# Kernel tuning notes

Hardware: AMD Instinct MI355X
Metric: run time of the kernel (lower is better)

The kernel has to match this reference:

```python
import jax, jax.numpy as jnp
import numpy as np
from jax import lax

B, C, H, W = 8, 64, 112, 112
MID = 256
K = 5
DIL = 2
PAD = 4


def setup_inputs() -> dict:
    key = jax.random.key(0)
    k1, k2, k3, k4, k5 = jax.random.split(key, 5)
    x = jax.random.normal(k1, (B, C, H, W), dtype=jnp.float32)
    # conv1: in_channel -> 256, k=5, dilation=2, pad=4
    w1 = jax.random.normal(k2, (MID, C, K, K), dtype=jnp.float32) * (1.0 / np.sqrt(C * K * K))
    b1 = jax.random.normal(k3, (MID,), dtype=jnp.float32) * 0.01
    # conv2: 256 -> 25, 1x1
    w2 = jax.random.normal(k4, (K * K, MID, 1, 1), dtype=jnp.float32) * (1.0 / np.sqrt(MID))
    b2 = jax.random.normal(k5, (K * K,), dtype=jnp.float32) * 0.01
    return {"x": x, "w1": w1, "b1": b1, "w2": w2, "b2": b2}


def reference(x, w1, b1, w2, b2):
    # attention-weight branch
    k = lax.conv_general_dilated(
        x, w1, window_strides=(1, 1), padding=[(PAD, PAD), (PAD, PAD)],
        rhs_dilation=(DIL, DIL), dimension_numbers=("NCHW", "OIHW", "NCHW"))
    k = k + b1[None, :, None, None]                       # [B, 256, H, W]
    k = jnp.einsum("oi,bihw->bohw", w2[:, :, 0, 0], k) + b2[None, :, None, None]
    k = jax.nn.softmax(k, axis=1)                          # [B, 25, H, W]

    # fused local attention: weighted sum over the 5x5 dilated neighborhood.
    # Equivalent to unfold(x, k=5, dilation=2, pad=4) * k summed over the 25 taps,
    # but never materializes the [B, C, 25, H, W] unfolded tensor.
    xp = jnp.pad(x, ((0, 0), (0, 0), (PAD, PAD), (PAD, PAD)))
    out = jnp.zeros_like(x)
    for idx in range(K * K):
        i, j = divmod(idx, K)
        patch = lax.dynamic_slice(xp, (0, 0, DIL * i, DIL * j), (B, C, H, W))
        out = out + patch * k[:, idx:idx + 1]              # broadcast over C
    return out
```

## Files before the change

kernel.cpp:

```cpp
#include <hip/hip_runtime.h>

#define BATCH 8
#define CH    64
#define HH    112
#define WW    112
#define HW    (HH * WW)
#define NP    (BATCH * HW)
#define TAPS  25
#define MIDC  256
#define PIX   64
#define CPW   16
#define NBLK  (NP / PIX)
#define NXCD  8
#define CPX   (NBLK / NXCD)

#define WEFF_N   (CH * TAPS * TAPS)
#define WEFF_TOT (WEFF_N + TAPS)
__global__ __launch_bounds__(256) void weff_kernel(
    const float* __restrict__ w1, const float* __restrict__ b1,
    const float* __restrict__ w2, const float* __restrict__ b2,
    float* __restrict__ weff, float* __restrict__ beff) {
  __shared__ float part[3][64];
  const int lane  = threadIdx.x & 63;
  const int chunk = threadIdx.x >> 6;
  const int id    = blockIdx.x * 64 + lane;

  float acc = 0.f;
  if (id < WEFF_N) {
    const int tap = id % TAPS;
    const int t2  = id / TAPS;
    const int o   = t2 % TAPS;
    const int c   = t2 / TAPS;
    const float* w2o = w2 + o * MIDC + chunk * 64;
    const float* w1p = w1 + ((size_t)(chunk * 64) * CH + c) * TAPS + tap;
    float a0 = 0.f, a1 = 0.f;
    #pragma unroll 8
    for (int m = 0; m < 64; m += 2) {
      a0 = fmaf(w1p[(size_t)m       * CH * TAPS], w2o[m],     a0);
      a1 = fmaf(w1p[(size_t)(m + 1) * CH * TAPS], w2o[m + 1], a1);
    }
    acc = a0 + a1;
  } else if (id < WEFF_TOT) {
    const int o = id - WEFF_N;
    const float* w2o = w2 + o * MIDC + chunk * 64;
    const float* b1p = b1 + chunk * 64;
    #pragma unroll 8
    for (int m = 0; m < 64; ++m) acc = fmaf(w2o[m], b1p[m], acc);
  }

  if (chunk) part[chunk - 1][lane] = acc;
  __syncthreads();
  if (chunk == 0 && id < WEFF_TOT) {
    float r = acc + part[0][lane] + part[1][lane] + part[2][lane];
    if (id < WEFF_N) {
      const int tap = id % TAPS;
      const int t2  = id / TAPS;
      const int o   = t2 % TAPS;
      const int c   = t2 / TAPS;
      weff[(c * TAPS + tap) * TAPS + o] = r;
    } else {
      beff[id - WEFF_N] = r + b2[id - WEFF_N];
    }
  }
}

__global__ __launch_bounds__(256, 6) void picanet_main(
    const float* __restrict__ x, const float* __restrict__ weff,
    const float* __restrict__ beff, float* __restrict__ out) {
  __shared__ float red[2 * PIX * TAPS];

  const int lane = threadIdx.x & 63;
  const int wave = threadIdx.x >> 6;
  const int c0 = __builtin_amdgcn_readfirstlane(wave * CPW);

  const int lb = (blockIdx.x & (NXCD - 1)) * CPX + (blockIdx.x >> 3);
  const int p  = lb * PIX + lane;
  const int b  = p / HW;
  const int hw = p % HW;
  const int h  = hw / WW;
  const int w  = hw % WW;

  const float* xb = x + (size_t)b * CH * HW + (size_t)c0 * HW;
  const float* wc = weff + (size_t)c0 * (TAPS * TAPS);

  float s[TAPS];
  #pragma unroll
  for (int o = 0; o < TAPS; ++o) s[o] = 0.f;

  #pragma unroll 1
  for (int tap = 0; tap < TAPS; ++tap) {
    int i = tap / 5, j = tap % 5;
    int yy = h + 2 * i - 4;
    int xx = w + 2 * j - 4;
    if (yy >= 0 && yy < HH && xx >= 0 && xx < WW) {
      const float* xp = xb + yy * WW + xx;
      float xv[CPW];
      #pragma unroll
      for (int c = 0; c < CPW; ++c) xv[c] = xp[(size_t)c * HW];
      const float* wt = wc + tap * TAPS;
      #pragma unroll
      for (int c = 0; c < CPW; ++c) {
        const float* wp = wt + c * (TAPS * TAPS);
        #pragma unroll
        for (int o = 0; o < TAPS; ++o) s[o] = fmaf(xv[c], wp[o], s[o]);
      }
    }
  }

  if (wave >= 2) {
    float* dst = red + (wave - 2) * (PIX * TAPS);
    #pragma unroll
    for (int o = 0; o < TAPS; ++o) dst[lane * TAPS + o] = s[o];
  }
  __syncthreads();
  if (wave < 2) {
    const float* srcp = red + wave * (PIX * TAPS);
    #pragma unroll
    for (int o = 0; o < TAPS; ++o) s[o] += srcp[lane * TAPS + o];
  }
  if (wave == 1) {
    float* dst = red + (PIX * TAPS);
    #pragma unroll
    for (int o = 0; o < TAPS; ++o) dst[lane * TAPS + o] = s[o];
  }
  __syncthreads();

  if (wave == 0) {
    const float* srcp = red + (PIX * TAPS);
    float t[TAPS];
    #pragma unroll
    for (int o = 0; o < TAPS; ++o)
      t[o] = s[o] + srcp[lane * TAPS + o] + beff[o];
    float m = t[0];
    #pragma unroll
    for (int o = 1; o < TAPS; ++o) m = fmaxf(m, t[o]);
    float sum = 0.f;
    #pragma unroll
    for (int o = 0; o < TAPS; ++o) { t[o] = __expf(t[o] - m); sum += t[o]; }
    float inv = 1.f / sum;
    #pragma unroll
    for (int o = 0; o < TAPS; ++o) red[lane * TAPS + o] = t[o] * inv;
  }
  __syncthreads();

  float acc[CPW];
  #pragma unroll
  for (int c = 0; c < CPW; ++c) acc[c] = 0.f;

  #pragma unroll 1
  for (int tap = 0; tap < TAPS; ++tap) {
    int i = tap / 5, j = tap % 5;
    int yy = h + 2 * i - 4;
    int xx = w + 2 * j - 4;
    float sv = red[lane * TAPS + tap];
    if (yy >= 0 && yy < HH && xx >= 0 && xx < WW) {
      const float* xp = xb + yy * WW + xx;
      #pragma unroll
      for (int c = 0; c < CPW; ++c)
        acc[c] = fmaf(sv, xp[(size_t)c * HW], acc[c]);
    }
  }

  float* ob = out + (size_t)b * CH * HW + (size_t)c0 * HW + hw;
  #pragma unroll
  for (int c = 0; c < CPW; ++c) ob[c * HW] = acc[c];
}

extern "C" void kernel_launch(void* const* d_in, const int* in_sizes, int n_in,
                              void* d_out, int out_size, void* d_ws, size_t ws_size,
                              hipStream_t stream) {
  const float* x  = (const float*)d_in[0];
  const float* w1 = (const float*)d_in[1];
  const float* b1 = (const float*)d_in[2];
  const float* w2 = (const float*)d_in[3];
  const float* b2 = (const float*)d_in[4];
  float* out  = (float*)d_out;
  float* weff = (float*)d_ws;
  float* beff = weff + WEFF_N;

  weff_kernel<<<(WEFF_TOT + 63) / 64, 256, 0, stream>>>(
      w1, b1, w2, b2, weff, beff);
  picanet_main<<<NBLK, 256, 0, stream>>>(x, weff, beff, out);
}
```

Measured before the change: 215.8 us.

## Share horizontal tap loads via wave shuffles and reorder weff by kernel row

The first-stage logit loop now goes over kernel rows. Each row needs two global loads per channel (the leftmost and rightmost column taps), and the three middle column taps come from cross-lane shuffles, since 64 consecutive pixels usually lie in one image row. The weff layout is reordered to [row][channel][col][o] so each row's weights are contiguous. This replaces five strided global loads per channel per row with two loads and six shuffles, at the cost of extra shuffle and select instructions and reliance on a tile layout in which shuffled neighbours are valid.

```diff
diff --git a/kernel.cpp b/kernel.cpp
--- a/kernel.cpp
+++ b/kernel.cpp
@@ -57,7 +57,8 @@
       const int t2  = id / TAPS;
       const int o   = t2 % TAPS;
       const int c   = t2 / TAPS;
-      weff[(c * TAPS + tap) * TAPS + o] = r;
+      const int ii  = tap / 5, jj = tap % 5;
+      weff[(((size_t)ii * CH + c) * 5 + jj) * TAPS + o] = r;
     } else {
       beff[id - WEFF_N] = r + b2[id - WEFF_N];
     }
@@ -81,29 +82,63 @@
   const int w  = hw % WW;
 
   const float* xb = x + (size_t)b * CH * HW + (size_t)c0 * HW;
-  const float* wc = weff + (size_t)c0 * (TAPS * TAPS);
+
+  bool colok[5];
+  #pragma unroll
+  for (int j = 0; j < 5; ++j) {
+    int xx = w + 2 * j - 4;
+    colok[j] = (xx >= 0) & (xx < WW);
+  }
+  const int a1 = lane + 2, a2 = lane + 4, a3 = lane + 6;
+  const int b1i = lane - 6, b2i = lane - 4, b3i = lane - 2;
 
   float s[TAPS];
   #pragma unroll
   for (int o = 0; o < TAPS; ++o) s[o] = 0.f;
 
   #pragma unroll 1
-  for (int tap = 0; tap < TAPS; ++tap) {
-    int i = tap / 5, j = tap % 5;
-    int yy = h + 2 * i - 4;
-    int xx = w + 2 * j - 4;
-    if (yy >= 0 && yy < HH && xx >= 0 && xx < WW) {
-      const float* xp = xb + yy * WW + xx;
-      float xv[CPW];
-      #pragma unroll
-      for (int c = 0; c < CPW; ++c) xv[c] = xp[(size_t)c * HW];
-      const float* wt = wc + tap * TAPS;
-      #pragma unroll
-      for (int c = 0; c < CPW; ++c) {
-        const float* wp = wt + c * (TAPS * TAPS);
-        #pragma unroll
-        for (int o = 0; o < TAPS; ++o) s[o] = fmaf(xv[c], wp[o], s[o]);
-      }
+  for (int i = 0; i < 5; ++i) {
+    const int dy  = 2 * i - 4;
+    const int yy  = h + dy;
+    const bool rowok = (yy >= 0) & (yy < HH);
+    if (!__any((int)rowok)) continue;
+
+    int ia = hw + dy * WW - 4;
+    int ib = hw + dy * WW + 4;
+    ia = min(max(ia, 0), HW - 1);
+    ib = min(max(ib, 0), HW - 1);
+
+    bool ok0 = rowok & colok[0], ok1 = rowok & colok[1];
+    bool ok2 = rowok & colok[2], ok3 = rowok & colok[3];
+    bool ok4 = rowok & colok[4];
+
+    const float* wci = weff + ((size_t)i * CH + c0) * (5 * TAPS);
+
+    #pragma unroll
+    for (int c = 0; c < CPW; ++c) {
+      const float A = xb[(size_t)c * HW + ia];
+      const float B = xb[(size_t)c * HW + ib];
+
+      float sA1 = __shfl(A, a1), sB1 = __shfl(B, b1i);
+      float sA2 = __shfl(A, a2), sB2 = __shfl(B, b2i);
+      float sA3 = __shfl(A, a3), sB3 = __shfl(B, b3i);
+      float v0 = ok0 ? A : 0.f;
+      float v1 = ok1 ? ((lane <= 61) ? sA1 : sB1) : 0.f;
+      float v2 = ok2 ? ((lane <= 59) ? sA2 : sB2) : 0.f;
+      float v3 = ok3 ? ((lane <= 57) ? sA3 : sB3) : 0.f;
+      float v4 = ok4 ? B : 0.f;
+
+      const float* wp = wci + c * (5 * TAPS);
+      #pragma unroll
+      for (int o = 0; o < TAPS; ++o) s[o] = fmaf(v0, wp[o],       s[o]);
+      #pragma unroll
+      for (int o = 0; o < TAPS; ++o) s[o] = fmaf(v1, wp[25 + o],  s[o]);
+      #pragma unroll
+      for (int o = 0; o < TAPS; ++o) s[o] = fmaf(v2, wp[50 + o],  s[o]);
+      #pragma unroll
+      for (int o = 0; o < TAPS; ++o) s[o] = fmaf(v3, wp[75 + o],  s[o]);
+      #pragma unroll
+      for (int o = 0; o < TAPS; ++o) s[o] = fmaf(v4, wp[100 + o], s[o]);
     }
   }
 
```

New measurement: 308.5 us. +42.9%, slower.

## Stage per-tap effective weights in LDS with register-prefetched double buffering

Applied to the files above, without the earlier changes.

Reorders the fused weight tensor to be tap-major and stages each tap's 64x25 weight slice into padded shared memory. The next tap's slice is prefetched into registers during the current tap's compute. This replaces wave-uniform scalar or global loads of weights in the inner loop with LDS reads. It adds two block barriers per tap and extra register and LDS pressure, which may lower occupancy under the 6-block launch bound.

```diff
diff --git a/kernel.cpp b/kernel.cpp
--- a/kernel.cpp
+++ b/kernel.cpp
@@ -13,6 +13,8 @@
 #define NBLK  (NP / PIX)
 #define NXCD  8
 #define CPX   (NBLK / NXCD)
+#define WTAP  (CH * TAPS)
+#define WPAD  28
 
 #define WEFF_N   (CH * TAPS * TAPS)
 #define WEFF_TOT (WEFF_N + TAPS)
@@ -57,7 +59,7 @@
       const int t2  = id / TAPS;
       const int o   = t2 % TAPS;
       const int c   = t2 / TAPS;
-      weff[(c * TAPS + tap) * TAPS + o] = r;
+      weff[((size_t)tap * CH + c) * TAPS + o] = r;
     } else {
       beff[id - WEFF_N] = r + b2[id - WEFF_N];
     }
@@ -67,10 +69,12 @@
 __global__ __launch_bounds__(256, 6) void picanet_main(
     const float* __restrict__ x, const float* __restrict__ weff,
     const float* __restrict__ beff, float* __restrict__ out) {
+  __shared__ float wlds[CH * WPAD];
   __shared__ float red[2 * PIX * TAPS];
 
-  const int lane = threadIdx.x & 63;
-  const int wave = threadIdx.x >> 6;
+  const int tid  = threadIdx.x;
+  const int lane = tid & 63;
+  const int wave = tid >> 6;
   const int c0 = __builtin_amdgcn_readfirstlane(wave * CPW);
 
   const int lb = (blockIdx.x & (NXCD - 1)) * CPX + (blockIdx.x >> 3);
@@ -81,7 +85,16 @@
   const int w  = hw % WW;
 
   const float* xb = x + (size_t)b * CH * HW + (size_t)c0 * HW;
-  const float* wc = weff + (size_t)c0 * (TAPS * TAPS);
+
+  {
+    const float* wg = weff;
+    #pragma unroll
+    for (int k = 0; k < 7; ++k) {
+      int e = tid + k * 256;
+      if (e < WTAP) { int c = e / 25, o = e - c * 25; wlds[c * WPAD + o] = wg[e]; }
+    }
+  }
+  __syncthreads();
 
   float s[TAPS];
   #pragma unroll
@@ -89,6 +102,16 @@
 
   #pragma unroll 1
   for (int tap = 0; tap < TAPS; ++tap) {
+    float pw[7];
+    if (tap < TAPS - 1) {
+      const float* wg = weff + (size_t)(tap + 1) * WTAP;
+      #pragma unroll
+      for (int k = 0; k < 7; ++k) {
+        int e = tid + k * 256;
+        pw[k] = (e < WTAP) ? wg[e] : 0.f;
+      }
+    }
+
     int i = tap / 5, j = tap % 5;
     int yy = h + 2 * i - 4;
     int xx = w + 2 * j - 4;
@@ -97,14 +120,23 @@
       float xv[CPW];
       #pragma unroll
       for (int c = 0; c < CPW; ++c) xv[c] = xp[(size_t)c * HW];
-      const float* wt = wc + tap * TAPS;
       #pragma unroll
       for (int c = 0; c < CPW; ++c) {
-        const float* wp = wt + c * (TAPS * TAPS);
+        const float* wp = wlds + (c0 + c) * WPAD;
         #pragma unroll
         for (int o = 0; o < TAPS; ++o) s[o] = fmaf(xv[c], wp[o], s[o]);
       }
     }
+
+    __syncthreads();
+    if (tap < TAPS - 1) {
+      #pragma unroll
+      for (int k = 0; k < 7; ++k) {
+        int e = tid + k * 256;
+        if (e < WTAP) { int c = e / 25, o = e - c * 25; wlds[c * WPAD + o] = pw[k]; }
+      }
+    }
+    __syncthreads();
   }
 
   if (wave >= 2) {
```

Measured after the change: 364.8 us. 69.0% more time.

## Stage per-tap effective weights in double-buffered LDS with register prefetch

Applied to the files above, without the earlier changes.

Relayouts the fused weight tensor to tap-major with a padded row of 28, then stages each tap's 64x28 weight slab into a double-buffered shared-memory area. The next tap's slab is prefetched into registers while the current one is used. This aims to replace repeated wave-uniform global/scalar weight loads with LDS reads shared across the block. It adds a block barrier per tap and extra LDS footprint, which may reduce overlap and occupancy.

```diff
diff --git a/kernel.cpp b/kernel.cpp
--- a/kernel.cpp
+++ b/kernel.cpp
@@ -13,9 +13,12 @@
 #define NBLK  (NP / PIX)
 #define NXCD  8
 #define CPX   (NBLK / NXCD)
+#define WPAD  28
+#define WSLAB (CH * WPAD)
 
 #define WEFF_N   (CH * TAPS * TAPS)
 #define WEFF_TOT (WEFF_N + TAPS)
+#define WEFF_PAD (TAPS * WSLAB)
 __global__ __launch_bounds__(256) void weff_kernel(
     const float* __restrict__ w1, const float* __restrict__ b1,
     const float* __restrict__ w2, const float* __restrict__ b2,
@@ -57,7 +60,7 @@
       const int t2  = id / TAPS;
       const int o   = t2 % TAPS;
       const int c   = t2 / TAPS;
-      weff[(c * TAPS + tap) * TAPS + o] = r;
+      weff[((size_t)tap * CH + c) * WPAD + o] = r;
     } else {
       beff[id - WEFF_N] = r + b2[id - WEFF_N];
     }
@@ -67,10 +70,12 @@
 __global__ __launch_bounds__(256, 6) void picanet_main(
     const float* __restrict__ x, const float* __restrict__ weff,
     const float* __restrict__ beff, float* __restrict__ out) {
-  __shared__ float red[2 * PIX * TAPS];
-
-  const int lane = threadIdx.x & 63;
-  const int wave = threadIdx.x >> 6;
+  __shared__ float pool[WSLAB + 2 * PIX * TAPS];
+  float* red = pool + WSLAB;
+
+  const int tid  = threadIdx.x;
+  const int lane = tid & 63;
+  const int wave = tid >> 6;
   const int c0 = __builtin_amdgcn_readfirstlane(wave * CPW);
 
   const int lb = (blockIdx.x & (NXCD - 1)) * CPX + (blockIdx.x >> 3);
@@ -81,14 +86,34 @@
   const int w  = hw % WW;
 
   const float* xb = x + (size_t)b * CH * HW + (size_t)c0 * HW;
-  const float* wc = weff + (size_t)c0 * (TAPS * TAPS);
 
   float s[TAPS];
   #pragma unroll
   for (int o = 0; o < TAPS; ++o) s[o] = 0.f;
 
+  float4 nv0, nv1;
+  {
+    const float4* wg4 = (const float4*)weff;
+    nv0 = wg4[tid];
+    nv1 = (tid < 192) ? wg4[256 + tid] : make_float4(0.f, 0.f, 0.f, 0.f);
+  }
+
   #pragma unroll 1
   for (int tap = 0; tap < TAPS; ++tap) {
+    const int sb = (tap & 1) * WSLAB;
+
+    {
+      float4* wl4 = (float4*)(pool + sb);
+      wl4[tid] = nv0;
+      if (tid < 192) wl4[256 + tid] = nv1;
+    }
+    if (tap < TAPS - 1) {
+      const float4* wg4 = (const float4*)(weff + (size_t)(tap + 1) * WSLAB);
+      nv0 = wg4[tid];
+      nv1 = (tid < 192) ? wg4[256 + tid] : make_float4(0.f, 0.f, 0.f, 0.f);
+    }
+    __syncthreads();
+
     int i = tap / 5, j = tap % 5;
     int yy = h + 2 * i - 4;
     int xx = w + 2 * j - 4;
@@ -97,10 +122,9 @@
       float xv[CPW];
       #pragma unroll
       for (int c = 0; c < CPW; ++c) xv[c] = xp[(size_t)c * HW];
-      const float* wt = wc + tap * TAPS;
       #pragma unroll
       for (int c = 0; c < CPW; ++c) {
-        const float* wp = wt + c * (TAPS * TAPS);
+        const float* wp = pool + sb + (c0 + c) * WPAD;
         #pragma unroll
         for (int o = 0; o < TAPS; ++o) s[o] = fmaf(xv[c], wp[o], s[o]);
       }
@@ -176,7 +200,7 @@
   const float* b2 = (const float*)d_in[4];
   float* out  = (float*)d_out;
   float* weff = (float*)d_ws;
-  float* beff = weff + WEFF_N;
+  float* beff = weff + WEFF_PAD;
 
   weff_kernel<<<(WEFF_TOT + 63) / 64, 256, 0, stream>>>(
       w1, b1, w2, b2, weff, beff);
```

Measured after the change: 283.1 us. 31.1% more time.
